# Performance work log

Measured on AMD Instinct MI355X. Metric: run time of the kernel, lower is better.

Reference implementation:

```python
import jax, jax.numpy as jnp
import numpy as np

B, T = 4, 2048
OBS, ST = 512, 512
H, E = 8, 64

def setup_inputs() -> dict:
    key = jax.random.key(0)
    k1, k2, k3, k4, k5 = jax.random.split(key, 5)
    observe = jax.random.normal(k1, (B, T, OBS), dtype=jnp.float32)
    state = jax.random.normal(k2, (B, T, ST), dtype=jnp.float32)
    # nn.Linear weights (out, in) applied as x @ W.T; store transposed for einsum
    Wq = jax.random.normal(k3, (OBS, H * E), dtype=jnp.float32) * (1.0 / np.sqrt(OBS))
    Wk = jax.random.normal(k4, (ST, H * E), dtype=jnp.float32) * (1.0 / np.sqrt(ST))
    Wv = jax.random.normal(k5, (ST, H * E), dtype=jnp.float32) * (1.0 / np.sqrt(ST))
    merge_w = jnp.ones((1, H, E), dtype=jnp.float32)  # Merger weight, init fill_(1.0)
    return {"observe": observe, "state": state, "Wq": Wq, "Wk": Wk, "Wv": Wv, "merge_w": merge_w}

def reference(observe, state, Wq, Wk, Wv, merge_w):
    b, t, _ = observe.shape
    h, e = H, E
    scale = e ** 0.25
    q = (observe @ Wq).reshape(b, t, h, e).transpose(0, 2, 1, 3) / scale  # [b,h,t,e]
    k = (state @ Wk).reshape(b, t, h, e).transpose(0, 2, 1, 3) / scale
    v = (state @ Wv).reshape(b, t, h, e).transpose(0, 2, 1, 3)
    dot = jnp.einsum('bhqe,bhke->bhqk', q, k)  # [b,h,t,t]
    attn = jax.nn.softmax(dot, axis=-1)
    out = jnp.einsum('bhqk,bhke->bhqe', attn, v)  # [b,h,t,e]
    out = out.transpose(0, 2, 1, 3).reshape(b * t, h, e)  # [b*t,h,e]
    # Merger: softmax over head dim of learned weight, weighted head sum
    w = jax.nn.softmax(merge_w, axis=1)  # [1,h,e]
    return jnp.sum(w * out, axis=1)  # [b*t,e]
```

## Files before the change

kernel.cpp:

```cpp
#include <hip/hip_runtime.h>

#define B_ 4
#define T_ 2048
#define H_ 8
#define E_ 64
#define KDIM 512

typedef unsigned short ushort_t;
typedef __attribute__((ext_vector_type(4))) float f32x4;
typedef __attribute__((ext_vector_type(4))) int i32x4;
typedef __attribute__((ext_vector_type(8))) short s16x8;

#define QK_SCALE 0.42466043f

__device__ __forceinline__ ushort_t f2bf(float f) {
  unsigned u = __builtin_bit_cast(unsigned, f);
  u += 0x7fffu + ((u >> 16) & 1u);
  return (ushort_t)(u >> 16);
}
__device__ __forceinline__ unsigned pk2(float a, float b) {
  return (unsigned)f2bf(a) | ((unsigned)f2bf(b) << 16);
}
__device__ __forceinline__ unsigned pk2t(float a, float b) {
  return __builtin_amdgcn_perm(__builtin_bit_cast(unsigned, b),
                               __builtin_bit_cast(unsigned, a), 0x07060302u);
}
__device__ __forceinline__ float e2(float x) { return __builtin_amdgcn_exp2f(x); }
__device__ __forceinline__ void gl2lds16(const void* g, void* l) {
  __builtin_amdgcn_global_load_lds((const __attribute__((address_space(1))) unsigned*)g,
                                   (__attribute__((address_space(3))) unsigned*)l, 16, 0, 0);
}

__global__ void k_prep(const float* __restrict__ Wq, const float* __restrict__ Wk,
                       const float* __restrict__ Wv, ushort_t* __restrict__ wt) {
  __shared__ ushort_t tile[64][66];
  int z = blockIdx.z;
  const float* W = (z == 0) ? Wq : (z == 1 ? Wk : Wv);
  float scale = (z < 2) ? QK_SCALE : 1.0f;
  int k0 = blockIdx.y << 6, n0 = blockIdx.x << 6;
  int rr = threadIdx.x >> 6, cc = threadIdx.x & 63;
  for (int p = 0; p < 16; p++) {
    int kl = p * 4 + rr;
    tile[cc][kl] = f2bf(W[(size_t)(k0 + kl) * 512 + n0 + cc] * scale);
  }
  __syncthreads();
  int kp2 = threadIdx.x & 31, nr = threadIdx.x >> 5;
  unsigned* wt32 = (unsigned*)(wt + (size_t)z * 262144);
  for (int p = 0; p < 8; p++) {
    int nl = p * 8 + nr;
    unsigned val = (unsigned)tile[nl][kp2 * 2] | ((unsigned)tile[nl][kp2 * 2 + 1] << 16);
    wt32[(size_t)(n0 + nl) * 256 + (k0 >> 1) + kp2] = val;
  }
}

__global__ void k_wgt(const float* __restrict__ mw, float* __restrict__ wgt) {
  int e = threadIdx.x;
  float w[8], wmax = -1e30f;
  for (int h = 0; h < 8; h++) { w[h] = mw[h * 64 + e]; wmax = fmaxf(wmax, w[h]); }
  float wsum = 0.f;
  for (int h = 0; h < 8; h++) { w[h] = __expf(w[h] - wmax); wsum += w[h]; }
  float inv = 1.f / wsum;
  for (int h = 0; h < 8; h++) wgt[h * 64 + e] = w[h] * inv;
}

__global__ __launch_bounds__(256, 2) void k_proj(
    const float* __restrict__ obs, const float* __restrict__ st,
    const ushort_t* __restrict__ wt,
    ushort_t* __restrict__ qo, ushort_t* __restrict__ ko, ushort_t* __restrict__ vto) {
  __shared__ __align__(16) float As[2][128 * 64];

  int id = blockIdx.x;
  int xcd = id & 7, nt = (id >> 3) & 3, ghi = id >> 5;
  int g = ghi * 8 + xcd;
  int which = g >> 6, mb = g & 63;
  int m0 = mb << 7, n0 = nt << 7;
  const float* X = (which == 0) ? obs : st;
  const ushort_t* W = wt + which * 262144;

  int tid = threadIdx.x, wave = tid >> 6, lane = tid & 63;
  int l15 = lane & 15, quad = lane >> 4;
  int wm = wave & 1, wn = wave >> 1;

  f32x4 acc[4][4];
  for (int i = 0; i < 4; i++)
    for (int j = 0; j < 4; j++) acc[i][j] = (f32x4){0.f, 0.f, 0.f, 0.f};

  int arl = lane >> 4, ap = lane & 15;

#define STAGEA(buf, k0)                                                          \
  do {                                                                           \
    for (int ii = 0; ii < 8; ii++) {                                             \
      int r = wave * 32 + ii * 4 + arl;                                          \
      int lc = ap ^ ((r & 7) << 1);                                              \
      gl2lds16(X + (size_t)(m0 + r) * KDIM + (k0) + lc * 4,                      \
               &As[buf][(wave * 32 + ii * 4) * 64]);                             \
    }                                                                            \
  } while (0)

  const ushort_t* wb[4];
  for (int j = 0; j < 4; j++)
    wb[j] = W + (size_t)(n0 + wn * 64 + j * 16 + l15) * KDIM + quad * 8;

  STAGEA(0, 0);
  __builtin_amdgcn_s_waitcnt(0x0F70);
  __syncthreads();

  for (int kt = 0; kt < 8; kt++) {
    s16x8 b[2][4];
    for (int kc = 0; kc < 2; kc++)
      for (int j = 0; j < 4; j++) b[kc][j] = *(const s16x8*)(wb[j] + kc * 32);
    for (int j = 0; j < 4; j++) wb[j] += 64;
    if (kt < 7) STAGEA((kt + 1) & 1, kt * 64 + 64);
    const float* asb = As[kt & 1];
    for (int kc = 0; kc < 2; kc++) {
      s16x8 a[4];
      for (int i = 0; i < 4; i++) {
        int mr = wm * 64 + i * 16 + l15;
        int pc = (kc * 8 + quad * 2) ^ ((l15 & 7) << 1);
        const float* ap2 = &asb[mr * 64 + pc * 4];
        float4 x0 = *(const float4*)ap2;
        float4 x1 = *(const float4*)(ap2 + 4);
        i32x4 d;
        d[0] = (int)pk2(x0.x, x0.y);
        d[1] = (int)pk2(x0.z, x0.w);
        d[2] = (int)pk2(x1.x, x1.y);
        d[3] = (int)pk2(x1.z, x1.w);
        a[i] = __builtin_bit_cast(s16x8, d);
      }
      if (which == 2) {
        for (int i = 0; i < 4; i++)
          for (int j = 0; j < 4; j++)
            acc[i][j] = __builtin_amdgcn_mfma_f32_16x16x32_bf16(b[kc][j], a[i], acc[i][j], 0, 0, 0);
      } else {
        for (int i = 0; i < 4; i++)
          for (int j = 0; j < 4; j++)
            acc[i][j] = __builtin_amdgcn_mfma_f32_16x16x32_bf16(a[i], b[kc][j], acc[i][j], 0, 0, 0);
      }
    }
    __builtin_amdgcn_s_waitcnt(0x0F70);
    __syncthreads();
  }
#undef STAGEA

  if (which != 2) {
    ushort_t* dst = (which == 0) ? qo : ko;
    for (int i = 0; i < 4; i++) {
      int grow = m0 + wm * 64 + i * 16 + quad * 4;
      for (int j = 0; j < 4; j++) {
        int gcol = n0 + wn * 64 + j * 16 + l15;
        int h = gcol >> 6, e = gcol & 63;
        for (int r = 0; r < 4; r++) {
          int row = grow + r;
          int bb = row >> 11, t = row & 2047;
          int bh = bb * H_ + h;
          dst[(((size_t)bh * T_ + t) << 6) + e] = f2bf(acc[i][j][r]);
        }
      }
    }
  } else {
    for (int i = 0; i < 4; i++) {
      int row = m0 + wm * 64 + i * 16 + l15;
      int bb = row >> 11, t = row & 2047;
      for (int j = 0; j < 4; j++) {
        for (int r = 0; r < 4; r++) {
          int gcol = n0 + wn * 64 + j * 16 + quad * 4 + r;
          int h = gcol >> 6, e = gcol & 63;
          int bh = bb * H_ + h;
          vto[((size_t)(bh << 6) + e) * T_ + t] = f2bf(acc[i][j][r]);
        }
      }
    }
  }
}

__global__ __launch_bounds__(256, 2) void k_attn(
    const ushort_t* __restrict__ q, const ushort_t* __restrict__ k,
    const ushort_t* __restrict__ vt, const float* __restrict__ wgt,
    float* __restrict__ out) {
  __shared__ __align__(16) ushort_t ks[2][128 * 64];
  __shared__ __align__(16) ushort_t vs[2][64 * 128];

  int id = blockIdx.x;
  int bh = id & 31, qt = id >> 5;
  int tid = threadIdx.x, wave = tid >> 6, lane = tid & 63;
  int l15 = lane & 15, quad = lane >> 4;

  s16x8 qf[2][2];
  for (int qs = 0; qs < 2; qs++) {
    const ushort_t* qp =
        q + (((size_t)bh * T_ + qt * 128 + wave * 32 + qs * 16 + l15) << 6) + quad * 8;
    qf[qs][0] = *(const s16x8*)qp;
    qf[qs][1] = *(const s16x8*)(qp + 32);
  }

  f32x4 o[2][4];
  for (int qs = 0; qs < 2; qs++)
    for (int j = 0; j < 4; j++) o[qs][j] = (f32x4){0.f, 0.f, 0.f, 0.f};
  f32x4 lacc[2] = {(f32x4){0.f, 0.f, 0.f, 0.f}, (f32x4){0.f, 0.f, 0.f, 0.f}};
  const s16x8 ones = {16256, 16256, 16256, 16256, 16256, 16256, 16256, 16256};

  int krl = lane >> 3, kp = lane & 7;
  int vrl = lane >> 4, vp = lane & 15;
  const ushort_t* kbase = k + ((size_t)bh * T_ << 6);
  const ushort_t* vbase = vt + ((size_t)bh << 6) * T_;
  const ushort_t* kptr[4];
  const ushort_t* vptr[4];
  for (int ii = 0; ii < 4; ii++) {
    int r = wave * 32 + ii * 8 + krl;
    int gkey = (r & 96) + (((r >> 2) & 3) << 3) + (((r >> 4) & 1) << 2) + (r & 3);
    int lc = kp ^ (r & 7);
    kptr[ii] = kbase + ((size_t)gkey << 6) + lc * 8;
    int e = wave * 16 + ii * 4 + vrl;
    int lcv = vp ^ (e & 15);
    vptr[ii] = vbase + (size_t)e * T_ + lcv * 8;
  }

#define STAGE(buf)                                                        \
  do {                                                                    \
    for (int ii = 0; ii < 4; ii++) {                                      \
      gl2lds16(kptr[ii], &ks[buf][(wave * 32 + ii * 8) * 64]);            \
      gl2lds16(vptr[ii], &vs[buf][(wave * 16 + ii * 4) * 128]);           \
      kptr[ii] += 128 * 64;                                               \
      vptr[ii] += 128;                                                    \
    }                                                                     \
  } while (0)

  STAGE(0);
  for (int kt = 0; kt < 16; kt++) {
    __builtin_amdgcn_s_waitcnt(0x0F70);
    __syncthreads();
    if (kt < 15) STAGE((kt + 1) & 1);
    const ushort_t* ksb = ks[kt & 1];
    const ushort_t* vsb = vs[kt & 1];

    s16x8 bfr[2][4];
    for (int c = 0; c < 4; c++) {
      f32x4 s0[2], s1[2];
      for (int qs = 0; qs < 2; qs++) {
        s0[qs] = (f32x4){0.f, 0.f, 0.f, 0.f};
        s1[qs] = (f32x4){0.f, 0.f, 0.f, 0.f};
      }
      for (int kc = 0; kc < 2; kc++) {
        int pc = (kc * 4 + quad) ^ (l15 & 7);
        s16x8 k0f = *(const s16x8*)&ksb[(c * 32 + l15) * 64 + pc * 8];
        s16x8 k1f = *(const s16x8*)&ksb[(c * 32 + 16 + l15) * 64 + pc * 8];
        for (int qs = 0; qs < 2; qs++) {
          s0[qs] = __builtin_amdgcn_mfma_f32_16x16x32_bf16(k0f, qf[qs][kc], s0[qs], 0, 0, 0);
          s1[qs] = __builtin_amdgcn_mfma_f32_16x16x32_bf16(k1f, qf[qs][kc], s1[qs], 0, 0, 0);
        }
      }
      for (int qs = 0; qs < 2; qs++) {
        i32x4 d;
        d[0] = (int)pk2t(e2(s0[qs][0]), e2(s0[qs][1]));
        d[1] = (int)pk2t(e2(s0[qs][2]), e2(s0[qs][3]));
        d[2] = (int)pk2t(e2(s1[qs][0]), e2(s1[qs][1]));
        d[3] = (int)pk2t(e2(s1[qs][2]), e2(s1[qs][3]));
        bfr[qs][c] = __builtin_bit_cast(s16x8, d);
      }
    }

    for (int c = 0; c < 4; c++) {
      lacc[0] = __builtin_amdgcn_mfma_f32_16x16x32_bf16(ones, bfr[0][c], lacc[0], 0, 0, 0);
      lacc[1] = __builtin_amdgcn_mfma_f32_16x16x32_bf16(ones, bfr[1][c], lacc[1], 0, 0, 0);
      for (int et = 0; et < 4; et++) {
        int pc = (c * 4 + quad) ^ l15;
        s16x8 vf = *(const s16x8*)&vsb[(et * 16 + l15) * 128 + pc * 8];
        o[0][et] = __builtin_amdgcn_mfma_f32_16x16x32_bf16(vf, bfr[0][c], o[0][et], 0, 0, 0);
        o[1][et] = __builtin_amdgcn_mfma_f32_16x16x32_bf16(vf, bfr[1][c], o[1][et], 0, 0, 0);
      }
    }
  }
#undef STAGE

  int bb = bh >> 3, hh = bh & 7;
  for (int qs = 0; qs < 2; qs++) {
    float inv = 1.f / lacc[qs][0];
    int t = qt * 128 + wave * 32 + qs * 16 + l15;
    for (int et = 0; et < 4; et++)
      for (int r = 0; r < 4; r++) {
        int e = et * 16 + quad * 4 + r;
        float val = o[qs][et][r] * inv * wgt[hh * 64 + e];
        atomicAdd(&out[(((size_t)bb * T_ + t) << 6) + e], val);
      }
  }
}

extern "C" void kernel_launch(void* const* d_in, const int* in_sizes, int n_in,
                              void* d_out, int out_size, void* d_ws, size_t ws_size,
                              hipStream_t stream) {
  const float* obs = (const float*)d_in[0];
  const float* st  = (const float*)d_in[1];
  const float* Wq  = (const float*)d_in[2];
  const float* Wk  = (const float*)d_in[3];
  const float* Wv  = (const float*)d_in[4];
  const float* mw  = (const float*)d_in[5];

  const size_t WS_NEEDED = 27262976;
  char* ws = (char*)d_ws;
  ushort_t* wt  = (ushort_t*)ws;
  float*    wgt = (float*)(ws + 1572864u);
  ushort_t* qo  = (ushort_t*)(ws + 2097152u);
  ushort_t* ko  = (ushort_t*)(ws + 10485760u);
  ushort_t* vto = (ushort_t*)(ws + 18874368u);
  float*    out = (float*)d_out;

  hipMemsetAsync(d_out, 0, (size_t)out_size * sizeof(float), stream);
  if (ws_size < WS_NEEDED) return;

  hipLaunchKernelGGL(k_prep, dim3(8, 8, 3), dim3(256), 0, stream, Wq, Wk, Wv, wt);
  hipLaunchKernelGGL(k_wgt,  dim3(1),       dim3(64),  0, stream, mw, wgt);
  hipLaunchKernelGGL(k_proj, dim3(768),     dim3(256), 0, stream, obs, st, wt, qo, ko, vto);
  hipLaunchKernelGGL(k_attn, dim3(512),     dim3(256), 0, stream, qo, ko, vto, wgt, out);
}
```

Before: 207.8 us.

## Halve LDS tiles in projection and attention, raise occupancy, coalesce atomic epilogue

The projection kernel now stages 32-wide K slices instead of 64, halving its LDS footprint, and asks for 3 blocks per CU. The attention kernel stages 64-key tiles instead of 128, so it runs twice as many loop iterations, and asks for 4 blocks per CU. Its epilogue now stages the output tile through a shared-memory union so that each wave issues atomicAdds across 64 contiguous elements instead of scattered strided ones. The aim is more resident waves to hide latency, plus coalesced atomics, at the cost of more barriers per tile and extra register pressure from the tighter launch bounds.

```diff
diff --git a/kernel.cpp b/kernel.cpp
--- a/kernel.cpp
+++ b/kernel.cpp
@@ -63,11 +63,11 @@
   for (int h = 0; h < 8; h++) wgt[h * 64 + e] = w[h] * inv;
 }
 
-__global__ __launch_bounds__(256, 2) void k_proj(
+__global__ __launch_bounds__(256, 3) void k_proj(
     const float* __restrict__ obs, const float* __restrict__ st,
     const ushort_t* __restrict__ wt,
     ushort_t* __restrict__ qo, ushort_t* __restrict__ ko, ushort_t* __restrict__ vto) {
-  __shared__ __align__(16) float As[2][128 * 64];
+  __shared__ __align__(16) float As[2][128 * 32];
 
   int id = blockIdx.x;
   int xcd = id & 7, nt = (id >> 3) & 3, ghi = id >> 5;
@@ -85,16 +85,15 @@
   for (int i = 0; i < 4; i++)
     for (int j = 0; j < 4; j++) acc[i][j] = (f32x4){0.f, 0.f, 0.f, 0.f};
 
-  int arl = lane >> 4, ap = lane & 15;
-
-#define STAGEA(buf, k0)                                                          \
-  do {                                                                           \
-    for (int ii = 0; ii < 8; ii++) {                                             \
-      int r = wave * 32 + ii * 4 + arl;                                          \
-      int lc = ap ^ ((r & 7) << 1);                                              \
-      gl2lds16(X + (size_t)(m0 + r) * KDIM + (k0) + lc * 4,                      \
-               &As[buf][(wave * 32 + ii * 4) * 64]);                             \
-    }                                                                            \
+  int arl = lane >> 3, ap = lane & 7;
+
+#define STAGEA(buf, k0)                                                           \
+  do {                                                                            \
+    for (int ii = 0; ii < 4; ii++) {                                              \
+      int r = wave * 32 + ii * 8 + arl;                                           \
+      gl2lds16(X + (size_t)(m0 + r) * KDIM + (k0) + ((ap ^ (r & 7)) << 2),        \
+               &As[buf][(wave * 32 + ii * 8) * 32]);                              \
+    }                                                                             \
   } while (0)
 
   const ushort_t* wb[4];
@@ -105,37 +104,33 @@
   __builtin_amdgcn_s_waitcnt(0x0F70);
   __syncthreads();
 
-  for (int kt = 0; kt < 8; kt++) {
-    s16x8 b[2][4];
-    for (int kc = 0; kc < 2; kc++)
-      for (int j = 0; j < 4; j++) b[kc][j] = *(const s16x8*)(wb[j] + kc * 32);
-    for (int j = 0; j < 4; j++) wb[j] += 64;
-    if (kt < 7) STAGEA((kt + 1) & 1, kt * 64 + 64);
+  for (int kt = 0; kt < 16; kt++) {
+    s16x8 b[4];
+    for (int j = 0; j < 4; j++) { b[j] = *(const s16x8*)wb[j]; wb[j] += 32; }
+    if (kt < 15) STAGEA((kt + 1) & 1, kt * 32 + 32);
     const float* asb = As[kt & 1];
-    for (int kc = 0; kc < 2; kc++) {
-      s16x8 a[4];
-      for (int i = 0; i < 4; i++) {
-        int mr = wm * 64 + i * 16 + l15;
-        int pc = (kc * 8 + quad * 2) ^ ((l15 & 7) << 1);
-        const float* ap2 = &asb[mr * 64 + pc * 4];
-        float4 x0 = *(const float4*)ap2;
-        float4 x1 = *(const float4*)(ap2 + 4);
-        i32x4 d;
-        d[0] = (int)pk2(x0.x, x0.y);
-        d[1] = (int)pk2(x0.z, x0.w);
-        d[2] = (int)pk2(x1.x, x1.y);
-        d[3] = (int)pk2(x1.z, x1.w);
-        a[i] = __builtin_bit_cast(s16x8, d);
-      }
-      if (which == 2) {
-        for (int i = 0; i < 4; i++)
-          for (int j = 0; j < 4; j++)
-            acc[i][j] = __builtin_amdgcn_mfma_f32_16x16x32_bf16(b[kc][j], a[i], acc[i][j], 0, 0, 0);
-      } else {
-        for (int i = 0; i < 4; i++)
-          for (int j = 0; j < 4; j++)
-            acc[i][j] = __builtin_amdgcn_mfma_f32_16x16x32_bf16(a[i], b[kc][j], acc[i][j], 0, 0, 0);
-      }
+    s16x8 a[4];
+    for (int i = 0; i < 4; i++) {
+      int mr = wm * 64 + i * 16 + l15;
+      int s = mr & 7;
+      const float* rowp = &asb[mr * 32];
+      float4 x0 = *(const float4*)&rowp[(((quad << 1)) ^ s) << 2];
+      float4 x1 = *(const float4*)&rowp[(((quad << 1) | 1) ^ s) << 2];
+      i32x4 d;
+      d[0] = (int)pk2(x0.x, x0.y);
+      d[1] = (int)pk2(x0.z, x0.w);
+      d[2] = (int)pk2(x1.x, x1.y);
+      d[3] = (int)pk2(x1.z, x1.w);
+      a[i] = __builtin_bit_cast(s16x8, d);
+    }
+    if (which == 2) {
+      for (int i = 0; i < 4; i++)
+        for (int j = 0; j < 4; j++)
+          acc[i][j] = __builtin_amdgcn_mfma_f32_16x16x32_bf16(b[j], a[i], acc[i][j], 0, 0, 0);
+    } else {
+      for (int i = 0; i < 4; i++)
+        for (int j = 0; j < 4; j++)
+          acc[i][j] = __builtin_amdgcn_mfma_f32_16x16x32_bf16(a[i], b[j], acc[i][j], 0, 0, 0);
     }
     __builtin_amdgcn_s_waitcnt(0x0F70);
     __syncthreads();
@@ -173,12 +168,16 @@
   }
 }
 
-__global__ __launch_bounds__(256, 2) void k_attn(
+union AttnSmem {
+  struct { ushort_t ks[2][64 * 64]; ushort_t vs[2][64 * 64]; } st;
+  struct { float ows[64 * 65]; float linv[64]; } ep;
+};
+
+__global__ __launch_bounds__(256, 4) void k_attn(
     const ushort_t* __restrict__ q, const ushort_t* __restrict__ k,
     const ushort_t* __restrict__ vt, const float* __restrict__ wgt,
     float* __restrict__ out) {
-  __shared__ __align__(16) ushort_t ks[2][128 * 64];
-  __shared__ __align__(16) ushort_t vs[2][64 * 128];
+  __shared__ __align__(16) AttnSmem sm;
 
   int id = blockIdx.x;
   int bh = id & 31, qt = id >> 5;
@@ -192,6 +191,8 @@
     qf[qs][0] = *(const s16x8*)qp;
     qf[qs][1] = *(const s16x8*)(qp + 32);
   }
+  int hh = bh & 7;
+  float wgl = wgt[hh * 64 + lane];
 
   f32x4 o[2][4];
   for (int qs = 0; qs < 2; qs++)
@@ -199,42 +200,39 @@
   f32x4 lacc[2] = {(f32x4){0.f, 0.f, 0.f, 0.f}, (f32x4){0.f, 0.f, 0.f, 0.f}};
   const s16x8 ones = {16256, 16256, 16256, 16256, 16256, 16256, 16256, 16256};
 
-  int krl = lane >> 3, kp = lane & 7;
-  int vrl = lane >> 4, vp = lane & 15;
+  int srl = lane >> 3, sp = lane & 7;
   const ushort_t* kbase = k + ((size_t)bh * T_ << 6);
   const ushort_t* vbase = vt + ((size_t)bh << 6) * T_;
-  const ushort_t* kptr[4];
-  const ushort_t* vptr[4];
-  for (int ii = 0; ii < 4; ii++) {
-    int r = wave * 32 + ii * 8 + krl;
-    int gkey = (r & 96) + (((r >> 2) & 3) << 3) + (((r >> 4) & 1) << 2) + (r & 3);
-    int lc = kp ^ (r & 7);
-    kptr[ii] = kbase + ((size_t)gkey << 6) + lc * 8;
-    int e = wave * 16 + ii * 4 + vrl;
-    int lcv = vp ^ (e & 15);
-    vptr[ii] = vbase + (size_t)e * T_ + lcv * 8;
-  }
-
-#define STAGE(buf)                                                        \
-  do {                                                                    \
-    for (int ii = 0; ii < 4; ii++) {                                      \
-      gl2lds16(kptr[ii], &ks[buf][(wave * 32 + ii * 8) * 64]);            \
-      gl2lds16(vptr[ii], &vs[buf][(wave * 16 + ii * 4) * 128]);           \
-      kptr[ii] += 128 * 64;                                               \
-      vptr[ii] += 128;                                                    \
-    }                                                                     \
+  const ushort_t* kptr[2];
+  const ushort_t* vptr[2];
+  for (int ii = 0; ii < 2; ii++) {
+    int r = wave * 16 + ii * 8 + srl;
+    int gkey = (r & 32) + (((r >> 2) & 3) << 3) + (((r >> 4) & 1) << 2) + (r & 3);
+    kptr[ii] = kbase + ((size_t)gkey << 6) + ((sp ^ (r & 7)) << 3);
+    int e = r;
+    vptr[ii] = vbase + (size_t)e * T_ + ((sp ^ (e & 7)) << 3);
+  }
+
+#define STAGE(buf)                                                         \
+  do {                                                                     \
+    for (int ii = 0; ii < 2; ii++) {                                       \
+      gl2lds16(kptr[ii], &sm.st.ks[buf][(wave * 16 + ii * 8) * 64]);       \
+      gl2lds16(vptr[ii], &sm.st.vs[buf][(wave * 16 + ii * 8) * 64]);       \
+      kptr[ii] += 64 * 64;                           \
+      vptr[ii] += 64;                  \
+    }                                                                      \
   } while (0)
 
   STAGE(0);
-  for (int kt = 0; kt < 16; kt++) {
+  for (int kt = 0; kt < 32; kt++) {
     __builtin_amdgcn_s_waitcnt(0x0F70);
     __syncthreads();
-    if (kt < 15) STAGE((kt + 1) & 1);
-    const ushort_t* ksb = ks[kt & 1];
-    const ushort_t* vsb = vs[kt & 1];
-
-    s16x8 bfr[2][4];
-    for (int c = 0; c < 4; c++) {
+    if (kt < 31) STAGE((kt + 1) & 1);
+    const ushort_t* ksb = sm.st.ks[kt & 1];
+    const ushort_t* vsb = sm.st.vs[kt & 1];
+
+    s16x8 bfr[2][2];
+    for (int c = 0; c < 2; c++) {
       f32x4 s0[2], s1[2];
       for (int qs = 0; qs < 2; qs++) {
         s0[qs] = (f32x4){0.f, 0.f, 0.f, 0.f};
@@ -259,12 +257,12 @@
       }
     }
 
-    for (int c = 0; c < 4; c++) {
+    for (int c = 0; c < 2; c++) {
       lacc[0] = __builtin_amdgcn_mfma_f32_16x16x32_bf16(ones, bfr[0][c], lacc[0], 0, 0, 0);
       lacc[1] = __builtin_amdgcn_mfma_f32_16x16x32_bf16(ones, bfr[1][c], lacc[1], 0, 0, 0);
       for (int et = 0; et < 4; et++) {
-        int pc = (c * 4 + quad) ^ l15;
-        s16x8 vf = *(const s16x8*)&vsb[(et * 16 + l15) * 128 + pc * 8];
+        int pc = (c * 4 + quad) ^ (l15 & 7);
+        s16x8 vf = *(const s16x8*)&vsb[(et * 16 + l15) * 64 + pc * 8];
         o[0][et] = __builtin_amdgcn_mfma_f32_16x16x32_bf16(vf, bfr[0][c], o[0][et], 0, 0, 0);
         o[1][et] = __builtin_amdgcn_mfma_f32_16x16x32_bf16(vf, bfr[1][c], o[1][et], 0, 0, 0);
       }
@@ -272,16 +270,26 @@
   }
 #undef STAGE
 
-  int bb = bh >> 3, hh = bh & 7;
-  for (int qs = 0; qs < 2; qs++) {
-    float inv = 1.f / lacc[qs][0];
-    int t = qt * 128 + wave * 32 + qs * 16 + l15;
-    for (int et = 0; et < 4; et++)
-      for (int r = 0; r < 4; r++) {
-        int e = et * 16 + quad * 4 + r;
-        float val = o[qs][et][r] * inv * wgt[hh * 64 + e];
-        atomicAdd(&out[(((size_t)bb * T_ + t) << 6) + e], val);
-      }
+  int bb = bh >> 3;
+  for (int half = 0; half < 2; half++) {
+    __syncthreads();
+    if ((wave >> 1) == half) {
+      int tl = (wave & 1) * 32;
+      for (int qs = 0; qs < 2; qs++) {
+        int row = tl + qs * 16 + l15;
+        if (quad == 0) sm.ep.linv[row] = 1.f / lacc[qs][0];
+        for (int et = 0; et < 4; et++)
+          for (int r = 0; r < 4; r++)
+            sm.ep.ows[row * 65 + et * 16 + quad * 4 + r] = o[qs][et][r];
+      }
+    }
+    __syncthreads();
+    for (int i = 0; i < 16; i++) {
+      int row = wave * 16 + i;
+      int gt = qt * 128 + half * 64 + row;
+      float val = sm.ep.ows[row * 65 + lane] * sm.ep.linv[row] * wgl;
+      atomicAdd(&out[(((size_t)bb * T_ + gt) << 6) + lane], val);
+    }
   }
 }
 
```

After: 194.0 us. 1.07x faster.
